# Kernel tuning notes

Measured on AMD Instinct MI355X. Metric: run time of the kernel, lower is better.

## Reference

```python
import jax, jax.numpy as jnp
import numpy as np

MARGIN = 0.5


def _pairwise_sqdist(a, b):
    # ||a_i - b_j||^2 = |a_i|^2 + |b_j|^2 - 2 a_i . b_j  -> [N, N]
    a2 = jnp.sum(a * a, axis=1)
    b2 = jnp.sum(b * b, axis=1)
    return a2[:, None] + b2[None, :] - 2.0 * (a @ b.T)


def setup_inputs() -> dict:
    key = jax.random.key(0)
    k1, k2 = jax.random.split(key)
    N, D = 4096, 256
    pair1 = jax.random.normal(k1, (N, D), dtype=jnp.float32)
    pair2 = jax.random.normal(k2, (N, D), dtype=jnp.float32)
    return {"pair1": pair1, "pair2": pair2}


def reference(pair1, pair2):
    N = pair1.shape[0]
    d11 = _pairwise_sqdist(pair1, pair1)          # dist(p1_i, p1_j)
    d12 = _pairwise_sqdist(pair1, pair2)          # dist(p1_i, p2_j)
    dist_ap = jnp.diagonal(d12)                   # ||p1_i - p2_i||^2, [N]
    off_diag = 1.0 - jnp.eye(N, dtype=pair1.dtype)  # exclude j == i
    hinge = (jax.nn.relu(dist_ap[:, None] - d11 + MARGIN)
             + jax.nn.relu(dist_ap[:, None] - d12 + MARGIN))
    losses = jnp.sum(hinge * off_diag)
    cnt = N * (N - 1)
    return losses / cnt
```

## Files before the change

kernel.cpp:

```cpp
#include <hip/hip_runtime.h>

#define NN 4096
#define DD 256
#define MARGIN 0.5f

typedef __attribute__((ext_vector_type(8))) short bf16x8;
typedef __attribute__((ext_vector_type(4))) float f32x4;

__device__ inline unsigned short f32_to_bf16_rne(float v) {
    unsigned int b = __float_as_uint(v);
    b += 0x7FFFu + ((b >> 16) & 1u);
    return (unsigned short)(b >> 16);
}

__global__ __launch_bounds__(256) void stats_convert(
    const float* __restrict__ p1, const float* __restrict__ p2,
    unsigned short* __restrict__ pb, float* __restrict__ nb,
    float* __restrict__ ai)
{
    const int wave = threadIdx.x >> 6;
    const int lane = threadIdx.x & 63;
    const int row  = blockIdx.x * 4 + wave;

    const float4 x = *(const float4*)&p1[(size_t)row * DD + lane * 4];
    const float4 y = *(const float4*)&p2[(size_t)row * DD + lane * 4];

    ushort4 xb, yb;
    xb.x = f32_to_bf16_rne(x.x); xb.y = f32_to_bf16_rne(x.y);
    xb.z = f32_to_bf16_rne(x.z); xb.w = f32_to_bf16_rne(x.w);
    yb.x = f32_to_bf16_rne(y.x); yb.y = f32_to_bf16_rne(y.y);
    yb.z = f32_to_bf16_rne(y.z); yb.w = f32_to_bf16_rne(y.w);
    *(ushort4*)&pb[(size_t)row * DD + lane * 4] = xb;
    *(ushort4*)&pb[(size_t)(NN + row) * DD + lane * 4] = yb;

    float s1 = x.x*x.x + x.y*x.y + x.z*x.z + x.w*x.w;
    float s2 = y.x*y.x + y.y*y.y + y.z*y.z + y.w*y.w;
    float dx = x.x-y.x, dy = x.y-y.y, dz = x.z-y.z, dw = x.w-y.w;
    float sa = dx*dx + dy*dy + dz*dz + dw*dw;

    #pragma unroll
    for (int off = 32; off > 0; off >>= 1) {
        s1 += __shfl_down(s1, off);
        s2 += __shfl_down(s2, off);
        sa += __shfl_down(sa, off);
    }
    if (lane == 0) {
        nb[row]      = s1;
        nb[NN + row] = s2;
        ai[row]      = sa - s1 + MARGIN;
    }
}

__global__ __launch_bounds__(256, 2) void gemm_hinge(
    const unsigned short* __restrict__ pb,
    const float* __restrict__ nb, const float* __restrict__ ai,
    float* __restrict__ partial)
{
    __shared__ unsigned short Bs[2][64 * 256];
    __shared__ float wsum[4];

    const int t    = threadIdx.x;
    const int lane = t & 63;
    const int wave = t >> 6;
    const int wm   = wave >> 1;
    const int wn   = wave & 1;

    const int bid     = blockIdx.x;
    const int istripe = (bid & 7) * 4 + (bid >> 7);
    const int jgroup  = (bid >> 3) & 15;
    const int i0      = istripe * 128;

    const int lr = lane & 15;
    const int l4 = lane >> 4;
    const int lk = l4 * 8;

    bf16x8 a[4][8];
    #pragma unroll
    for (int m = 0; m < 4; ++m) {
        const unsigned short* ar = pb + (size_t)(i0 + wm * 64 + m * 16 + lr) * DD;
        #pragma unroll
        for (int kq = 0; kq < 8; ++kq)
            a[m][kq] = *(const bf16x8*)(ar + kq * 32 + lk);
    }

    const int r0 = l4 * 4;
    float aiv[4][4];
    #pragma unroll
    for (int m = 0; m < 4; ++m)
        #pragma unroll
        for (int r = 0; r < 4; ++r)
            aiv[m][r] = ai[i0 + wm * 64 + m * 16 + r0 + r];

    auto stage = [&](int sel, int jt) {
        const unsigned short* base = pb + (size_t)jt * 64 * DD;
        #pragma unroll
        for (int q = 0; q < 8; ++q) {
            const int c   = q * 256 + t;
            const int row = c >> 5;
            const int cw  = c & 31;
            const unsigned short* g = base + row * DD + ((cw ^ (row & 7)) * 8);
            __builtin_amdgcn_global_load_lds(
                (const __attribute__((address_space(1))) unsigned int*)g,
                (__attribute__((address_space(3))) unsigned int*)
                    &Bs[sel][(q * 256 + wave * 64) * 8],
                16, 0, 0);
        }
    };

    const int jt0 = jgroup * 8;
    float lsum = 0.f;

    stage(0, jt0);
    __syncthreads();

    int sel = 0;
    for (int jj = 0; jj < 8; ++jj) {
        const int j0 = (jt0 + jj) * 64;
        if (jj < 7) stage(sel ^ 1, jt0 + jj + 1);

        f32x4 acc[4][2];
        #pragma unroll
        for (int m = 0; m < 4; ++m)
            #pragma unroll
            for (int n = 0; n < 2; ++n)
                acc[m][n] = (f32x4){0.f, 0.f, 0.f, 0.f};

        #pragma unroll
        for (int kq = 0; kq < 8; ++kq) {
            bf16x8 b[2];
            #pragma unroll
            for (int n = 0; n < 2; ++n) {
                const int row = wn * 32 + n * 16 + lr;
                const int cl  = kq * 4 + l4;
                b[n] = *(const bf16x8*)&Bs[sel][row * 256 + ((cl ^ (row & 7)) * 8)];
            }
            #pragma unroll
            for (int m = 0; m < 4; ++m)
                #pragma unroll
                for (int n = 0; n < 2; ++n)
                    acc[m][n] = __builtin_amdgcn_mfma_f32_16x16x32_bf16(
                        a[m][kq], b[n], acc[m][n], 0, 0, 0);
        }

        #pragma unroll
        for (int n = 0; n < 2; ++n) {
            const int j     = j0 + wn * 32 + n * 16 + lr;
            const float nbj = nb[j];
            #pragma unroll
            for (int m = 0; m < 4; ++m) {
                #pragma unroll
                for (int r = 0; r < 4; ++r) {
                    const int i = i0 + wm * 64 + m * 16 + r0 + r;
                    float h = fmaf(2.f, acc[m][n][r], aiv[m][r] - nbj);
                    h = fmaxf(h, 0.f);
                    if (j != i && j != i + NN) lsum += h;
                }
            }
        }

        __syncthreads();
        sel ^= 1;
    }

    #pragma unroll
    for (int off = 32; off > 0; off >>= 1) lsum += __shfl_down(lsum, off);
    if (lane == 0) wsum[wave] = lsum;
    __syncthreads();
    if (t == 0)
        partial[bid] = wsum[0] + wsum[1] + wsum[2] + wsum[3];
}

__global__ __launch_bounds__(256) void final_reduce(
    const float* __restrict__ partial, float* __restrict__ out,
    int n, float scale)
{
    const int t = threadIdx.x;
    float s = 0.f;
    for (int i = t; i < n; i += 256) s += partial[i];
    #pragma unroll
    for (int off = 32; off > 0; off >>= 1) s += __shfl_down(s, off);
    __shared__ float w[4];
    if ((t & 63) == 0) w[t >> 6] = s;
    __syncthreads();
    if (t == 0) out[0] = (w[0] + w[1] + w[2] + w[3]) * scale;
}

extern "C" void kernel_launch(void* const* d_in, const int* in_sizes, int n_in,
                              void* d_out, int out_size, void* d_ws, size_t ws_size,
                              hipStream_t stream) {
    const float* p1 = (const float*)d_in[0];
    const float* p2 = (const float*)d_in[1];
    float* out = (float*)d_out;

    char* ws = (char*)d_ws;
    unsigned short* pb = (unsigned short*)ws;
    float* nb      = (float*)(ws + (size_t)2 * NN * DD * 2);
    float* ai      = nb + 2 * NN;
    float* partial = ai + NN;

    stats_convert<<<NN / 4, 256, 0, stream>>>(p1, p2, pb, nb, ai);
    gemm_hinge<<<512, 256, 0, stream>>>(pb, nb, ai, partial);
    const float scale = 1.0f / ((float)NN * (float)(NN - 1));
    final_reduce<<<1, 256, 0, stream>>>(partial, out, 512, scale);
}
```

Before: 36.41 us.

## Drop diagonal masking via precomputed corrections and fuse final reduce with atomic counter

The per-element diagonal mask in the GEMM epilogue is removed. The diagonal hinge terms are instead computed in stats_convert, using bf16-rounded dot products so they match what the MFMA path produces, and subtracted at the end. The separate final_reduce launch is replaced by a last-block-done pattern: an atomic counter with threadfences, where the last block sums the partials and corrections. This saves epilogue compares and one kernel launch, at the cost of atomics and a serial tail in one block. The subtracted corrections may not exactly match what the MFMA accumulation computed for those entries.

```diff
diff --git a/kernel.cpp b/kernel.cpp
--- a/kernel.cpp
+++ b/kernel.cpp
@@ -12,12 +12,18 @@
     b += 0x7FFFu + ((b >> 16) & 1u);
     return (unsigned short)(b >> 16);
 }
+__device__ inline float bf16_to_f32(unsigned short u) {
+    return __uint_as_float(((unsigned int)u) << 16);
+}
 
 __global__ __launch_bounds__(256) void stats_convert(
     const float* __restrict__ p1, const float* __restrict__ p2,
     unsigned short* __restrict__ pb, float* __restrict__ nb,
-    float* __restrict__ ai)
+    float* __restrict__ ai, float* __restrict__ corr,
+    unsigned int* __restrict__ ctr)
 {
+    if (blockIdx.x == 0 && threadIdx.x == 0) *ctr = 0u;
+
     const int wave = threadIdx.x >> 6;
     const int lane = threadIdx.x & 63;
     const int row  = blockIdx.x * 4 + wave;
@@ -38,26 +44,40 @@
     float dx = x.x-y.x, dy = x.y-y.y, dz = x.z-y.z, dw = x.w-y.w;
     float sa = dx*dx + dy*dy + dz*dz + dw*dw;
 
+    float xf0 = bf16_to_f32(xb.x), xf1 = bf16_to_f32(xb.y),
+          xf2 = bf16_to_f32(xb.z), xf3 = bf16_to_f32(xb.w);
+    float yf0 = bf16_to_f32(yb.x), yf1 = bf16_to_f32(yb.y),
+          yf2 = bf16_to_f32(yb.z), yf3 = bf16_to_f32(yb.w);
+    float s1b  = xf0*xf0 + xf1*xf1 + xf2*xf2 + xf3*xf3;
+    float s12b = xf0*yf0 + xf1*yf1 + xf2*yf2 + xf3*yf3;
+
     #pragma unroll
     for (int off = 32; off > 0; off >>= 1) {
-        s1 += __shfl_down(s1, off);
-        s2 += __shfl_down(s2, off);
-        sa += __shfl_down(sa, off);
+        s1  += __shfl_down(s1,  off);
+        s2  += __shfl_down(s2,  off);
+        sa  += __shfl_down(sa,  off);
+        s1b += __shfl_down(s1b, off);
+        s12b+= __shfl_down(s12b,off);
     }
     if (lane == 0) {
         nb[row]      = s1;
         nb[NN + row] = s2;
         ai[row]      = sa - s1 + MARGIN;
+        const float t1 = fmaxf(sa - 2.f*s1 + MARGIN + 2.f*s1b, 0.f);
+        const float t2 = fmaxf(sa - s1 - s2 + MARGIN + 2.f*s12b, 0.f);
+        corr[row] = t1 + t2;
     }
 }
 
 __global__ __launch_bounds__(256, 2) void gemm_hinge(
     const unsigned short* __restrict__ pb,
     const float* __restrict__ nb, const float* __restrict__ ai,
-    float* __restrict__ partial)
+    const float* __restrict__ corr, float* __restrict__ partial,
+    unsigned int* __restrict__ ctr, float* __restrict__ out, float scale)
 {
     __shared__ unsigned short Bs[2][64 * 256];
     __shared__ float wsum[4];
+    __shared__ int is_last;
 
     const int t    = threadIdx.x;
     const int lane = t & 63;
@@ -144,18 +164,12 @@
 
         #pragma unroll
         for (int n = 0; n < 2; ++n) {
-            const int j     = j0 + wn * 32 + n * 16 + lr;
-            const float nbj = nb[j];
-            #pragma unroll
-            for (int m = 0; m < 4; ++m) {
+            const float nbj = nb[j0 + wn * 32 + n * 16 + lr];
+            #pragma unroll
+            for (int m = 0; m < 4; ++m)
                 #pragma unroll
-                for (int r = 0; r < 4; ++r) {
-                    const int i = i0 + wm * 64 + m * 16 + r0 + r;
-                    float h = fmaf(2.f, acc[m][n][r], aiv[m][r] - nbj);
-                    h = fmaxf(h, 0.f);
-                    if (j != i && j != i + NN) lsum += h;
-                }
-            }
+                for (int r = 0; r < 4; ++r)
+                    lsum += fmaxf(fmaf(2.f, acc[m][n][r], aiv[m][r] - nbj), 0.f);
         }
 
         __syncthreads();
@@ -166,23 +180,26 @@
     for (int off = 32; off > 0; off >>= 1) lsum += __shfl_down(lsum, off);
     if (lane == 0) wsum[wave] = lsum;
     __syncthreads();
-    if (t == 0)
+    if (t == 0) {
         partial[bid] = wsum[0] + wsum[1] + wsum[2] + wsum[3];
-}
-
-__global__ __launch_bounds__(256) void final_reduce(
-    const float* __restrict__ partial, float* __restrict__ out,
-    int n, float scale)
-{
-    const int t = threadIdx.x;
-    float s = 0.f;
-    for (int i = t; i < n; i += 256) s += partial[i];
-    #pragma unroll
-    for (int off = 32; off > 0; off >>= 1) s += __shfl_down(s, off);
-    __shared__ float w[4];
-    if ((t & 63) == 0) w[t >> 6] = s;
+        __threadfence();
+        unsigned int prev = atomicAdd(ctr, 1u);
+        is_last = (prev == 511u);
+    }
     __syncthreads();
-    if (t == 0) out[0] = (w[0] + w[1] + w[2] + w[3]) * scale;
+
+    if (is_last) {
+        __threadfence();
+        float s = 0.f;
+        for (int i = t; i < 512; i += 256) s += partial[i];
+        for (int i = t; i < NN; i += 256) s -= corr[i];
+        #pragma unroll
+        for (int off = 32; off > 0; off >>= 1) s += __shfl_down(s, off);
+        if (lane == 0) wsum[wave] = s;
+        __syncthreads();
+        if (t == 0)
+            out[0] = (wsum[0] + wsum[1] + wsum[2] + wsum[3]) * scale;
+    }
 }
 
 extern "C" void kernel_launch(void* const* d_in, const int* in_sizes, int n_in,
@@ -196,10 +213,11 @@
     unsigned short* pb = (unsigned short*)ws;
     float* nb      = (float*)(ws + (size_t)2 * NN * DD * 2);
     float* ai      = nb + 2 * NN;
-    float* partial = ai + NN;
-
-    stats_convert<<<NN / 4, 256, 0, stream>>>(p1, p2, pb, nb, ai);
-    gemm_hinge<<<512, 256, 0, stream>>>(pb, nb, ai, partial);
+    float* corr    = ai + NN;
+    float* partial = corr + NN;
+    unsigned int* ctr = (unsigned int*)(partial + 512);
     const float scale = 1.0f / ((float)NN * (float)(NN - 1));
-    final_reduce<<<1, 256, 0, stream>>>(partial, out, 512, scale);
-}
+
+    stats_convert<<<NN / 4, 256, 0, stream>>>(p1, p2, pb, nb, ai, corr, ctr);
+    gemm_hinge<<<512, 256, 0, stream>>>(pb, nb, ai, corr, partial, ctr, out, scale);
+}
```

Result: slower. 46.48 us (+27.7%).
